# Performance work log

Hardware: AMD Instinct MI355X
Metric: run time of the kernel (lower is better)

The kernel has to match this reference:

```python
import jax, jax.numpy as jnp
import numpy as np

HIDDEN = 1024
FFN = 2048
NUM_EXPERTS = 16
JITTER_EPS = 0.01


def setup_inputs() -> dict:
    key = jax.random.key(0)
    k1, k2, k3, k4 = jax.random.split(key, 4)
    hidden_states = jax.random.normal(k1, (4, 2048, HIDDEN), dtype=jnp.float32)
    gate_weight = jax.random.normal(k2, (NUM_EXPERTS, HIDDEN), dtype=jnp.float32) * 0.02
    # gate_up_weights[e, :FFN] = w1 (gate proj), [FFN:] = w3 (up proj)
    gate_up_weights = jax.random.normal(k3, (NUM_EXPERTS, 2 * FFN, HIDDEN), dtype=jnp.float32) * 0.02
    down_weights = jax.random.normal(k4, (NUM_EXPERTS, HIDDEN, FFN), dtype=jnp.float32) * 0.02
    return {
        'hidden_states': hidden_states,
        'gate_weight': gate_weight,
        'gate_up_weights': gate_up_weights,
        'down_weights': down_weights,
    }


def sparsemixer(scores, jitter_eps):
    # top-1 selection with jitter mask
    m1 = jnp.max(scores, axis=-1, keepdims=True)              # [T,1]
    ind1 = jnp.argmax(scores, axis=-1, keepdims=True)         # [T,1]
    factor1 = jnp.maximum(jnp.abs(scores), m1)
    mask1 = (m1 - scores) / factor1 > 2.0 * jitter_eps
    gates1 = jax.nn.softmax(jnp.where(mask1, -jnp.inf, scores), axis=-1)
    w1 = jnp.take_along_axis(gates1, ind1, axis=-1)           # [T,1]

    # mask out top-1, select top-2
    top1_onehot = jax.nn.one_hot(ind1[:, 0], scores.shape[-1], dtype=bool)
    masked_scores = jnp.where(top1_onehot, -jnp.inf, scores)
    m2 = jnp.max(masked_scores, axis=-1, keepdims=True)
    ind2 = jnp.argmax(masked_scores, axis=-1, keepdims=True)
    factor2 = jnp.maximum(jnp.abs(scores), m2)
    mask2 = (m2 - scores) / factor2 > 2.0 * jitter_eps
    gates2 = jax.nn.softmax(jnp.where(mask2, -jnp.inf, masked_scores), axis=-1)
    w2 = jnp.take_along_axis(gates2, ind2, axis=-1)           # [T,1]

    multipliers = jnp.concatenate([w1, w2], axis=-1)          # [T,2]
    experts = jnp.concatenate([ind1, ind2], axis=-1)          # [T,2] int
    return multipliers, experts


def fused_moe(x, gate_up_weights, down_weights, routing_weights, selected_experts):
    # x: [T,H], gate_up: [E,2F,H], down: [E,H,F]
    E = gate_up_weights.shape[0]
    ffn = down_weights.shape[2]
    # combine[t,e] = sum_k routing_weights[t,k] * (selected[t,k]==e)
    onehot = jax.nn.one_hot(selected_experts, E, dtype=x.dtype)     # [T,2,E]
    combine = jnp.einsum('tk,tke->te', routing_weights, onehot)     # [T,E]
    out = jnp.zeros_like(x)
    for e in range(E):
        gu = x @ gate_up_weights[e].T                                # [T,2F]
        h = jax.nn.silu(gu[:, :ffn]) * gu[:, ffn:]                   # [T,F]
        out = out + combine[:, e:e + 1] * (h @ down_weights[e].T)    # [T,H]
    return out


def reference(hidden_states, gate_weight, gate_up_weights, down_weights):
    B, S, H = hidden_states.shape
    x = hidden_states.reshape(-1, H)                         # [T,H]
    router_logits = x @ gate_weight.T                        # [T,E]
    routing_weights, selected_experts = sparsemixer(router_logits, JITTER_EPS)
    out = fused_moe(x, gate_up_weights, down_weights, routing_weights, selected_experts)
    return out.reshape(B, S, H), router_logits
```

## Files before the change

kernel.cpp:

```cpp
#include <hip/hip_runtime.h>
#include <hip/hip_bf16.h>
#include <math.h>

#define T_TOKENS 8192
#define HID 1024
#define FFN 2048
#define NEXP 16
#define NPAIR (2*T_TOKENS)
#define TM 128
#define MAXTILES 144

typedef short bf16x8 __attribute__((ext_vector_type(8)));
typedef float f32x4 __attribute__((ext_vector_type(4)));

static const size_t HPACK_OFF = 0;
static const size_t HPACK_SZ  = (size_t)MAXTILES * 32 * 16384;
static const size_t GPACK_OFF = HPACK_OFF + HPACK_SZ;
static const size_t GPACK_SZ  = (size_t)16 * 64 * 16 * 8192;
static const size_t DPACK_OFF = GPACK_OFF + GPACK_SZ;
static const size_t DPACK_SZ  = (size_t)16 * 16 * 32 * 8192;
static const size_t APACK_OFF = DPACK_OFF + DPACK_SZ;
static const size_t APACK_SZ  = (size_t)MAXTILES * 16 * 16384;
static const size_t WTK_OFF   = APACK_OFF + APACK_SZ;
static const size_t ETK_OFF   = WTK_OFF  + (size_t)NPAIR*4;
static const size_t RANK_OFF  = ETK_OFF  + (size_t)NPAIR*4;
static const size_t LIST_OFF  = RANK_OFF + (size_t)NPAIR*4;
static const size_t CNT_OFF   = LIST_OFF + (size_t)NPAIR*4;
static const size_t OFFS_OFF  = CNT_OFF  + 64;
static const size_t TEXP_OFF  = OFFS_OFF + 128;
static const size_t TSEG_OFF  = TEXP_OFF + (size_t)MAXTILES*4;
static const size_t HDR_OFF   = TSEG_OFF + (size_t)MAXTILES*4;

__device__ __forceinline__ unsigned short f2bf(float f) {
  union { float f; unsigned u; } v; v.f = f;
  unsigned r = v.u + 0x7fff + ((v.u >> 16) & 1);
  return (unsigned short)(r >> 16);
}

__device__ __forceinline__ bf16x8 pack8(float4 a, float4 b) {
  bf16x8 r;
  r[0]=(short)f2bf(a.x); r[1]=(short)f2bf(a.y); r[2]=(short)f2bf(a.z); r[3]=(short)f2bf(a.w);
  r[4]=(short)f2bf(b.x); r[5]=(short)f2bf(b.y); r[6]=(short)f2bf(b.z); r[7]=(short)f2bf(b.w);
  return r;
}

__device__ __forceinline__ void ld16(const unsigned short* g, unsigned short* l) {
  __builtin_amdgcn_global_load_lds((const __attribute__((address_space(1))) void*)g,
                                   (__attribute__((address_space(3))) void*)l, 16, 0, 0);
}

#define WAITV4 do { asm volatile("s_waitcnt vmcnt(4)" ::: "memory"); } while (0)
#define WAITV0 do { asm volatile("s_waitcnt vmcnt(0)" ::: "memory"); } while (0)
#define WAITL0 do { asm volatile("s_waitcnt lgkmcnt(0)" ::: "memory"); __builtin_amdgcn_sched_barrier(0); } while (0)
#define XBAR   do { __builtin_amdgcn_s_barrier(); __builtin_amdgcn_sched_barrier(0); } while (0)

__device__ __forceinline__ void pack_body(const float* __restrict__ src, unsigned short* __restrict__ dst,
                                          int e, int nb, int kb, int nbcnt, int kbcnt, int kdim,
                                          unsigned short* tile ) {
  int tid = threadIdx.x;
  int n = tid >> 2, ks = (tid & 3) * 16;
  const float* s = src + ((size_t)((e*nbcnt + nb)*64 + n))*kdim + kb*64 + ks;
  float4 f0 = *(const float4*)(s);
  float4 f1 = *(const float4*)(s + 4);
  float4 f2 = *(const float4*)(s + 8);
  float4 f3 = *(const float4*)(s + 12);
  int kkc0 = ks >> 3;
  *(bf16x8*)&tile[(kkc0*64 + n)*8]     = pack8(f0, f1);
  *(bf16x8*)&tile[((kkc0+1)*64 + n)*8] = pack8(f2, f3);
  __syncthreads();
  unsigned short* d = dst + ((size_t)(e*nbcnt + nb)*kbcnt + kb)*4096 + tid*16;
  *(bf16x8*)(d)     = *(const bf16x8*)&tile[tid*16];
  *(bf16x8*)(d + 8) = *(const bf16x8*)&tile[tid*16 + 8];
}

__global__ __launch_bounds__(256) void k_logits(const float* __restrict__ x,
                                                const float* __restrict__ gw,
                                                float* __restrict__ logits) {
  int tid = threadIdx.x;
  int wave = tid >> 6, lane = tid & 63;
  int t = blockIdx.x * 4 + wave;
  const float* xp = x + (size_t)t * HID;
  float acc[NEXP];
  #pragma unroll
  for (int e = 0; e < NEXP; e++) acc[e] = 0.f;
  for (int i = lane; i < HID; i += 64) {
    float xv = xp[i];
    #pragma unroll
    for (int e = 0; e < NEXP; e++) acc[e] += xv * gw[e*HID + i];
  }
  float mine = 0.f;
  #pragma unroll
  for (int e = 0; e < NEXP; e++) {
    float v = acc[e];
    #pragma unroll
    for (int o = 32; o > 0; o >>= 1) v += __shfl_xor(v, o, 64);
    if (lane == e) mine = v;
  }
  if (lane < NEXP) logits[(size_t)t*NEXP + lane] = mine;
}

__global__ __launch_bounds__(256) void k_route(const float* __restrict__ logits,
                                               float* __restrict__ wtk, int* __restrict__ etk,
                                               int* __restrict__ rank, int* __restrict__ counts) {
  int t = blockIdx.x*256 + threadIdx.x;
  if (t >= T_TOKENS) return;
  float s[NEXP];
  const float* lp = logits + (size_t)t*NEXP;
  #pragma unroll
  for (int e = 0; e < NEXP; e++) s[e] = lp[e];

  float m1 = s[0]; int i1 = 0;
  #pragma unroll
  for (int e = 1; e < NEXP; e++) if (s[e] > m1) { m1 = s[e]; i1 = e; }
  float sum1 = 0.f;
  #pragma unroll
  for (int e = 0; e < NEXP; e++) {
    float f = fmaxf(fabsf(s[e]), m1);
    if (!((m1 - s[e]) > 0.02f*f)) sum1 += expf(s[e]-m1);
  }
  float m2 = -INFINITY; int i2 = 0;
  #pragma unroll
  for (int e = 0; e < NEXP; e++) if (e != i1 && s[e] > m2) { m2 = s[e]; i2 = e; }
  float sum2 = 0.f;
  #pragma unroll
  for (int e = 0; e < NEXP; e++) {
    if (e == i1) continue;
    float f = fmaxf(fabsf(s[e]), m2);
    if (!((m2 - s[e]) > 0.02f*f)) sum2 += expf(s[e]-m2);
  }
  wtk[t*2]   = 1.f/sum1;
  wtk[t*2+1] = 1.f/sum2;
  etk[t*2]   = i1;
  etk[t*2+1] = i2;
  rank[t*2]   = atomicAdd(&counts[i1], 1);
  rank[t*2+1] = atomicAdd(&counts[i2], 1);
}

__global__ void k_scan(const int* __restrict__ counts, int* __restrict__ offsets,
                       int* __restrict__ texp, int* __restrict__ tseg, int* __restrict__ hdr) {
  if (threadIdx.x != 0 || blockIdx.x != 0) return;
  int off = 0, nt = 0;
  for (int e = 0; e < NEXP; e++) {
    offsets[e] = off;
    int c = counts[e];
    int tiles = (c + TM - 1)/TM;
    for (int i = 0; i < tiles; i++) { texp[nt] = e; tseg[nt] = i; nt++; }
    off += c;
  }
  offsets[NEXP] = off;
  hdr[0] = nt;
}

__global__ __launch_bounds__(256) void k_scatter(const int* __restrict__ etk,
                                                 const int* __restrict__ rank,
                                                 const int* __restrict__ offsets,
                                                 int* __restrict__ list) {
  int p = blockIdx.x*256 + threadIdx.x;
  if (p >= NPAIR) return;
  int e = etk[p];
  list[offsets[e] + rank[p]] = p;
}

__global__ __launch_bounds__(256) void k_prep(const float* __restrict__ gup,
                                              unsigned short* __restrict__ gpack,
                                              const float* __restrict__ x,
                                              const int* __restrict__ list,
                                              const int* __restrict__ counts,
                                              const int* __restrict__ offsets,
                                              const int* __restrict__ texp,
                                              const int* __restrict__ tseg,
                                              const int* __restrict__ hdr,
                                              unsigned short* __restrict__ apack) {
  __shared__ __align__(16) unsigned short tile[4096];
  int bid = blockIdx.x;
  if (bid < 16384) {
    int kb = bid & 15, nb = (bid >> 4) & 63, e = bid >> 10;
    pack_body(gup, gpack, e, nb, kb, 64, 16, HID, tile);
    return;
  }
  int by = bid - 16384;
  if (by >= hdr[0]) return;
  int e = texp[by];
  int m0 = tseg[by]*TM;
  int seg0 = offsets[e];
  int cnt = counts[e];
  int* toks = (int*)tile;
  int tid = threadIdx.x;
  if (tid < TM) toks[tid] = list[seg0 + min(m0 + tid, cnt-1)] >> 1;
  __syncthreads();
  #pragma unroll 4
  for (int it = 0; it < 64; ++it) {
    int flat = it*256 + tid;
    int kb = flat >> 10;
    int i  = flat & 1023;
    int kkc = i >> 7, row = i & 127;
    const float* s = x + (size_t)toks[row]*HID + kb*64 + kkc*8;
    float4 f0 = *(const float4*)(s);
    float4 f1 = *(const float4*)(s + 4);
    *(bf16x8*)(apack + ((size_t)(by*16 + kb))*8192 + (size_t)i*8) = pack8(f0, f1);
  }
}

__global__ __launch_bounds__(256,4) void k_gateup(const unsigned short* __restrict__ apack,
                                                  const unsigned short* __restrict__ gpack,
                                                  const float* __restrict__ dwn,
                                                  unsigned short* __restrict__ dpack,
                                                  const float* __restrict__ wtk,
                                                  const int* __restrict__ list,
                                                  const int* __restrict__ counts,
                                                  const int* __restrict__ offsets,
                                                  const int* __restrict__ texp,
                                                  const int* __restrict__ tseg,
                                                  const int* __restrict__ hdr,
                                                  unsigned short* __restrict__ hpack) {
  __shared__ __align__(16) unsigned short A_lds[2][4096];
  __shared__ __align__(16) unsigned short Bg_lds[2][2048];
  __shared__ __align__(16) unsigned short Bu_lds[2][2048];
  int bid = blockIdx.x;
  if (bid >= 4608) {
    int p = bid - 4608;
    pack_body(dwn, dpack, p >> 9, (p >> 5) & 15, p & 31, 16, 32, FFN, &A_lds[0][0]);
    return;
  }
  int fb = bid & 31;
  int by = bid >> 5;
  if (by >= hdr[0]) return;
  int e = texp[by];
  int m0 = tseg[by]*TM;
  int seg0 = offsets[e];
  int cnt = counts[e];
  int rows = min(TM, cnt - m0);

  int tid = threadIdx.x;
  int wid = tid >> 6, lane = tid & 63;
  int wr = wid >> 1, wc = wid & 1;
  int c4 = lane >> 4, r16 = lane & 15;

  const unsigned short* gA = apack + (size_t)by * 131072;
  const unsigned short* gG = gpack + ((size_t)(e*64 + fb))      * 65536;
  const unsigned short* gU = gpack + ((size_t)(e*64 + 32 + fb)) * 65536;

  f32x4 accg[4][2] = {};
  f32x4 accu[4][2] = {};

  auto STAGE = [&](int buf, int kb) {
    #pragma unroll
    for (int s = 0; s < 4; ++s) {
      int i = wid*4 + s;
      if (i < 8) {
        ld16(gA + (size_t)kb*4096 + i*512 + lane*8, &A_lds[buf][i*512]);
      } else if (i < 12) {
        int j = i - 8;
        ld16(gG + (size_t)kb*2048 + j*512 + lane*8, &Bg_lds[buf][j*512]);
      } else {
        int j = i - 12;
        ld16(gU + (size_t)kb*2048 + j*512 + lane*8, &Bu_lds[buf][j*512]);
      }
    }
  };

  auto COMPUTE = [&](int buf) {
    bf16x8 a[4], bg[2], bu[2];
    #pragma unroll
    for (int sm = 0; sm < 4; ++sm)
      a[sm] = *(const bf16x8*)&A_lds[buf][(c4*128 + wr*64 + sm*16 + r16)*8];
    #pragma unroll
    for (int sn = 0; sn < 2; ++sn) {
      bg[sn] = *(const bf16x8*)&Bg_lds[buf][(c4*64 + wc*32 + sn*16 + r16)*8];
      bu[sn] = *(const bf16x8*)&Bu_lds[buf][(c4*64 + wc*32 + sn*16 + r16)*8];
    }
    #pragma unroll
    for (int sm = 0; sm < 4; ++sm)
      #pragma unroll
      for (int sn = 0; sn < 2; ++sn) {
        accg[sm][sn] = __builtin_amdgcn_mfma_f32_16x16x32_bf16(a[sm], bg[sn], accg[sm][sn], 0, 0, 0);
        accu[sm][sn] = __builtin_amdgcn_mfma_f32_16x16x32_bf16(a[sm], bu[sn], accu[sm][sn], 0, 0, 0);
      }
  };

  STAGE(0, 0);
  STAGE(1, 1);
  int cur = 0;
  for (int kb = 0; kb < 31; ++kb) {
    WAITV4; XBAR;
    COMPUTE(cur);
    WAITL0; XBAR;
    if (kb < 30) STAGE(cur, kb + 2);
    cur ^= 1;
  }
  WAITV0; XBAR;
  COMPUTE(cur);
  __syncthreads();

  unsigned short* scr = &A_lds[0][0];
  #pragma unroll
  for (int sm = 0; sm < 4; ++sm) {
    #pragma unroll
    for (int j = 0; j < 4; ++j) {
      int row = wr*64 + sm*16 + (lane>>4)*4 + j;
      float w = (row < rows) ? wtk[list[seg0 + m0 + row]] : 0.f;
      #pragma unroll
      for (int sn = 0; sn < 2; ++sn) {
        int col = wc*32 + sn*16 + (lane & 15);
        float g = accg[sm][sn][j];
        float u = accu[sm][sn][j];
        float hv = g / (1.f + __expf(-g)) * u * w;
        scr[((col>>3)*128 + row)*8 + (col&7)] = f2bf(hv);
      }
    }
  }
  __syncthreads();
  unsigned short* dst = hpack + ((size_t)(by*32 + fb))*8192 + tid*32;
  const unsigned short* srcl = scr + tid*32;
  #pragma unroll
  for (int q = 0; q < 4; ++q)
    *(bf16x8*)(dst + q*8) = *(const bf16x8*)(srcl + q*8);
}

__global__ __launch_bounds__(256,4) void k_down(const unsigned short* __restrict__ hpack,
                                                const unsigned short* __restrict__ dpack,
                                                const int* __restrict__ counts,
                                                const int* __restrict__ texp,
                                                const int* __restrict__ tseg,
                                                const int* __restrict__ offsets,
                                                const int* __restrict__ hdr,
                                                float* __restrict__ ydown) {
  int nb = blockIdx.x;
  int by = blockIdx.y;
  if (by >= hdr[0]) return;
  int e = texp[by];
  int m0 = tseg[by]*TM;
  int seg0 = offsets[e];
  int cnt = counts[e];
  int rows = min(TM, cnt - m0);

  __shared__ __align__(16) unsigned short A_lds[2][4096];
  __shared__ __align__(16) unsigned short B_lds[2][4096];

  int tid = threadIdx.x;
  int wid = tid >> 6, lane = tid & 63;
  int wr = wid >> 1, wc = wid & 1;
  int c4 = lane >> 4, r16 = lane & 15;

  const unsigned short* hA = hpack + (size_t)by * 262144;

  f32x4 acc[4][4] = {};

  auto STAGE = [&](int buf, int kb) {
    #pragma unroll
    for (int s = 0; s < 4; ++s) {
      int i = wid*4 + s;
      if (i < 8) {
        ld16(hA + (size_t)kb*4096 + i*512 + lane*8, &A_lds[buf][i*512]);
      } else {
        int i2 = i - 8;
        int p = i2 >> 2, j = i2 & 3;
        ld16(dpack + (((size_t)(e*16 + nb*2 + p))*32 + (kb>>1))*4096 + (kb&1)*2048 + j*512 + lane*8,
             &B_lds[buf][p*2048 + j*512]);
      }
    }
  };

  auto COMPUTE = [&](int buf) {
    bf16x8 a[4], b[4];
    #pragma unroll
    for (int sm = 0; sm < 4; ++sm)
      a[sm] = *(const bf16x8*)&A_lds[buf][(c4*128 + wr*64 + sm*16 + r16)*8];
    #pragma unroll
    for (int sn = 0; sn < 4; ++sn) {
      int col = wc*64 + sn*16 + r16;
      b[sn] = *(const bf16x8*)&B_lds[buf][(col>>6)*2048 + (c4*64 + (col&63))*8];
    }
    #pragma unroll
    for (int sm = 0; sm < 4; ++sm)
      #pragma unroll
      for (int sn = 0; sn < 4; ++sn)
        acc[sm][sn] = __builtin_amdgcn_mfma_f32_16x16x32_bf16(a[sm], b[sn], acc[sm][sn], 0, 0, 0);
  };

  STAGE(0, 0);
  STAGE(1, 1);
  int cur = 0;
  for (int kb = 0; kb < 63; ++kb) {
    WAITV4; XBAR;
    COMPUTE(cur);
    WAITL0; XBAR;
    if (kb < 62) STAGE(cur, kb + 2);
    cur ^= 1;
  }
  WAITV0; XBAR;
  COMPUTE(cur);

  #pragma unroll
  for (int sm = 0; sm < 4; ++sm) {
    #pragma unroll
    for (int j = 0; j < 4; ++j) {
      int row = wr*64 + sm*16 + (lane>>4)*4 + j;
      if (row < rows) {
        size_t slot = (size_t)(seg0 + m0 + row);
        #pragma unroll
        for (int sn = 0; sn < 4; ++sn) {
          int col = nb*128 + wc*64 + sn*16 + r16;
          ydown[slot*HID + col] = acc[sm][sn][j];
        }
      }
    }
  }
}

__global__ __launch_bounds__(256) void k_final(const float* __restrict__ ydown,
                                               const int* __restrict__ etk,
                                               const int* __restrict__ rank,
                                               const int* __restrict__ offsets,
                                               float* __restrict__ out) {
  int t = blockIdx.x;
  int c = threadIdx.x;
  int p0 = t*2, p1 = t*2 + 1;
  int s0 = offsets[etk[p0]] + rank[p0];
  int s1 = offsets[etk[p1]] + rank[p1];
  float4 a = *(const float4*)(ydown + (size_t)s0*HID + c*4);
  float4 b = *(const float4*)(ydown + (size_t)s1*HID + c*4);
  float4 r; r.x = a.x+b.x; r.y = a.y+b.y; r.z = a.z+b.z; r.w = a.w+b.w;
  *(float4*)(out + (size_t)t*HID + c*4) = r;
}

extern "C" void kernel_launch(void* const* d_in, const int* in_sizes, int n_in,
                              void* d_out, int out_size, void* d_ws, size_t ws_size,
                              hipStream_t stream) {
  const float* x   = (const float*)d_in[0];
  const float* gw  = (const float*)d_in[1];
  const float* gup = (const float*)d_in[2];
  const float* dwn = (const float*)d_in[3];

  float* out = (float*)d_out;
  float* logits = out + (size_t)T_TOKENS*HID;

  char* ws = (char*)d_ws;
  unsigned short* hpack = (unsigned short*)(ws + HPACK_OFF);
  unsigned short* gpack = (unsigned short*)(ws + GPACK_OFF);
  unsigned short* dpack = (unsigned short*)(ws + DPACK_OFF);
  unsigned short* apack = (unsigned short*)(ws + APACK_OFF);
  float* ydown = (float*)(ws + GPACK_OFF);
  float* wtk   = (float*)(ws + WTK_OFF);
  int* etk     = (int*)(ws + ETK_OFF);
  int* rank    = (int*)(ws + RANK_OFF);
  int* list    = (int*)(ws + LIST_OFF);
  int* counts  = (int*)(ws + CNT_OFF);
  int* offsets = (int*)(ws + OFFS_OFF);
  int* texp    = (int*)(ws + TEXP_OFF);
  int* tseg    = (int*)(ws + TSEG_OFF);
  int* hdr     = (int*)(ws + HDR_OFF);

  hipMemsetAsync(counts, 0, 64, stream);

  k_logits<<<T_TOKENS/4, 256, 0, stream>>>(x, gw, logits);
  k_route<<<T_TOKENS/256, 256, 0, stream>>>(logits, wtk, etk, rank, counts);
  k_scan<<<1, 64, 0, stream>>>(counts, offsets, texp, tseg, hdr);
  k_scatter<<<NPAIR/256, 256, 0, stream>>>(etk, rank, offsets, list);

  k_prep<<<16384 + MAXTILES, 256, 0, stream>>>(gup, gpack, x, list, counts, offsets, texp, tseg, hdr, apack);

  k_gateup<<<4608 + 8192, 256, 0, stream>>>(apack, gpack, dwn, dpack, wtk, list, counts, offsets,
                                            texp, tseg, hdr, hpack);

  dim3 g4(8, MAXTILES);
  k_down<<<g4, 256, 0, stream>>>(hpack, dpack, counts, texp, tseg, offsets, hdr, ydown);

  k_final<<<T_TOKENS, 256, 0, stream>>>(ydown, etk, rank, offsets, out);
}
```

Before: 508.8 us.

## Triple-buffer LDS in gate-up and down GEMMs to drop one barrier per k-step

Both grouped GEMM kernels move from double to triple LDS buffering. The next stage load is issued before computing on the current buffer, so each k-iteration needs one barrier instead of two and loads overlap compute longer. The extra shared memory lowers the launch-bounds occupancy hint from 4 to 3 blocks per CU, which may reduce latency hiding across blocks.

```diff
diff --git a/kernel.cpp b/kernel.cpp
--- a/kernel.cpp
+++ b/kernel.cpp
@@ -201,7 +201,7 @@
   }
 }
 
-__global__ __launch_bounds__(256,4) void k_gateup(const unsigned short* __restrict__ apack,
+__global__ __launch_bounds__(256,3) void k_gateup(const unsigned short* __restrict__ apack,
                                                   const unsigned short* __restrict__ gpack,
                                                   const float* __restrict__ dwn,
                                                   unsigned short* __restrict__ dpack,
@@ -213,9 +213,9 @@
                                                   const int* __restrict__ tseg,
                                                   const int* __restrict__ hdr,
                                                   unsigned short* __restrict__ hpack) {
-  __shared__ __align__(16) unsigned short A_lds[2][4096];
-  __shared__ __align__(16) unsigned short Bg_lds[2][2048];
-  __shared__ __align__(16) unsigned short Bu_lds[2][2048];
+  __shared__ __align__(16) unsigned short A_lds[3][4096];
+  __shared__ __align__(16) unsigned short Bg_lds[3][2048];
+  __shared__ __align__(16) unsigned short Bu_lds[3][2048];
   int bid = blockIdx.x;
   if (bid >= 4608) {
     int p = bid - 4608;
@@ -280,15 +280,19 @@
 
   STAGE(0, 0);
   STAGE(1, 1);
-  int cur = 0;
+  int cur = 0, stg = 2;
   for (int kb = 0; kb < 31; ++kb) {
-    WAITV4; XBAR;
+    WAITL0;
+    WAITV4;
+    XBAR;
+    if (kb < 30) STAGE(stg, kb + 2);
     COMPUTE(cur);
-    WAITL0; XBAR;
-    if (kb < 30) STAGE(cur, kb + 2);
-    cur ^= 1;
-  }
-  WAITV0; XBAR;
+    cur = (cur == 2) ? 0 : cur + 1;
+    stg = (stg == 2) ? 0 : stg + 1;
+  }
+  WAITL0;
+  WAITV0;
+  XBAR;
   COMPUTE(cur);
   __syncthreads();
 
@@ -317,7 +321,7 @@
     *(bf16x8*)(dst + q*8) = *(const bf16x8*)(srcl + q*8);
 }
 
-__global__ __launch_bounds__(256,4) void k_down(const unsigned short* __restrict__ hpack,
+__global__ __launch_bounds__(256,3) void k_down(const unsigned short* __restrict__ hpack,
                                                 const unsigned short* __restrict__ dpack,
                                                 const int* __restrict__ counts,
                                                 const int* __restrict__ texp,
@@ -334,8 +338,8 @@
   int cnt = counts[e];
   int rows = min(TM, cnt - m0);
 
-  __shared__ __align__(16) unsigned short A_lds[2][4096];
-  __shared__ __align__(16) unsigned short B_lds[2][4096];
+  __shared__ __align__(16) unsigned short A_lds[3][4096];
+  __shared__ __align__(16) unsigned short B_lds[3][4096];
 
   int tid = threadIdx.x;
   int wid = tid >> 6, lane = tid & 63;
@@ -380,15 +384,19 @@
 
   STAGE(0, 0);
   STAGE(1, 1);
-  int cur = 0;
+  int cur = 0, stg = 2;
   for (int kb = 0; kb < 63; ++kb) {
-    WAITV4; XBAR;
+    WAITL0;
+    WAITV4;
+    XBAR;
+    if (kb < 62) STAGE(stg, kb + 2);
     COMPUTE(cur);
-    WAITL0; XBAR;
-    if (kb < 62) STAGE(cur, kb + 2);
-    cur ^= 1;
-  }
-  WAITV0; XBAR;
+    cur = (cur == 2) ? 0 : cur + 1;
+    stg = (stg == 2) ? 0 : stg + 1;
+  }
+  WAITL0;
+  WAITV0;
+  XBAR;
   COMPUTE(cur);
 
   #pragma unroll
```

Result: no change. 511.8 us (+0.6%).
